# Optimization experiments

Measured on AMD Instinct MI355X. Metric: run time of the kernel, lower is better.

Reference implementation:

```python
import jax, jax.numpy as jnp
import numpy as np

MSA_DIM = 256
NO_HEADS = 8
HIDDEN_DIM = 32
NORM_FACTOR = 1.0 / np.sqrt(HIDDEN_DIM)


def setup_inputs() -> dict:
    key = jax.random.key(0)
    ks = jax.random.split(key, 9)
    S, L, C = 256, 384, MSA_DIM
    HD = NO_HEADS * HIDDEN_DIM
    scale = 1.0 / np.sqrt(C)
    return {
        "msa_embed": jax.random.normal(ks[0], (S, L, C), dtype=jnp.float32),
        "ln_gamma": jnp.ones((C,), dtype=jnp.float32),
        "ln_beta": jnp.zeros((C,), dtype=jnp.float32),
        "wq": jax.random.normal(ks[1], (C, HD), dtype=jnp.float32) * scale,
        "wk": jax.random.normal(ks[2], (C, HD), dtype=jnp.float32) * scale,
        "wv": jax.random.normal(ks[3], (C, HD), dtype=jnp.float32) * scale,
        "wg": jax.random.normal(ks[4], (C, HD), dtype=jnp.float32) * scale,
        "bg": jnp.zeros((HD,), dtype=jnp.float32),
        "wo": jax.random.normal(ks[5], (HD, C), dtype=jnp.float32) * (1.0 / np.sqrt(HD)),
        "bo": jnp.zeros((C,), dtype=jnp.float32),
    }


def _layernorm(x, gamma, beta, eps=1e-5):
    mu = jnp.mean(x, axis=-1, keepdims=True)
    var = jnp.mean(jnp.square(x - mu), axis=-1, keepdims=True)
    return (x - mu) * jax.lax.rsqrt(var + eps) * gamma + beta


def reference(msa_embed, ln_gamma, ln_beta, wq, wk, wv, wg, bg, wo, bo):
    S, L, C = msa_embed.shape
    H, D = NO_HEADS, HIDDEN_DIM
    m = _layernorm(msa_embed, ln_gamma, ln_beta)
    q = (m @ wq).reshape(S, L, H, D) * NORM_FACTOR  # [S, L, H, D]
    k = (m @ wk).reshape(S, L, H, D)
    v = (m @ wv).reshape(S, L, H, D)
    # column attention: attend over the seq (S) axis, per column c
    attn = jnp.einsum('ichd,jchd->hcij', q, k)  # [H, L, S, S]
    attn = jax.nn.softmax(attn, axis=-1)
    gate = jax.nn.sigmoid(m @ wg + bg).reshape(S, L, H, D)
    out = jnp.einsum('hcij,jchd->ichd', attn, v) * gate  # [S, L, H, D]
    out = out.reshape(S, L, H * D)
    return out @ wo + bo
```

## Files before the change

### kernel.cpp

```cpp
#include <hip/hip_runtime.h>
#include <hip/hip_bf16.h>
#include <stdint.h>

#define NS 256
#define NL 384
#define NC 256
#define NH 8
#define ND 32
#define NHD 256
#define NFQ 0.17677669529663687f
#define QSCALE (NFQ * 1.4426950408889634f)

typedef unsigned short u16;
typedef unsigned int u32;
typedef __attribute__((ext_vector_type(8))) short short8;
typedef __attribute__((ext_vector_type(4))) float f32x4;

__device__ __forceinline__ float bf2f(u16 u) {
  union { u32 u; float f; } w; w.u = ((u32)u) << 16; return w.f;
}
__device__ __forceinline__ float lo16(u32 u) {
  union { u32 u; float f; } w; w.u = u << 16; return w.f;
}
__device__ __forceinline__ float hi16(u32 u) {
  union { u32 u; float f; } w; w.u = u & 0xffff0000u; return w.f;
}
__device__ __forceinline__ u16 f2bf_rne(float f) {
  u32 x = __float_as_uint(f);
  u32 lsb = (x >> 16) & 1u;
  x += 0x7fffu + lsb;
  return (u16)(x >> 16);
}
__device__ __forceinline__ u32 pk2(float a, float b) {
  u32 r;
  asm("v_cvt_pk_bf16_f32 %0, %1, %2" : "=v"(r) : "v"(a), "v"(b));
  return r;
}

__device__ __forceinline__ void gl_lds16(const u16* g, u16* l) {
  __builtin_amdgcn_global_load_lds(
      (const __attribute__((address_space(1))) void*)g,
      (__attribute__((address_space(3))) void*)l, 16, 0, 0);
}

template<bool F32>
__device__ __forceinline__ float ldE(const void* p, size_t i) {
  if constexpr (F32) return ((const float*)p)[i];
  else               return bf2f(((const u16*)p)[i]);
}
template<bool F32>
__device__ __forceinline__ void ld16(const void* p, size_t i, float* x) {
  if constexpr (F32) {
    const float4* q = (const float4*)((const float*)p + i);
#pragma unroll
    for (int w = 0; w < 4; ++w) {
      float4 v = q[w];
      x[4*w] = v.x; x[4*w+1] = v.y; x[4*w+2] = v.z; x[4*w+3] = v.w;
    }
  } else {
    const uint4* q = (const uint4*)((const u16*)p + i);
#pragma unroll
    for (int w = 0; w < 2; ++w) {
      uint4 v = q[w];
      u32 uu[4] = {v.x, v.y, v.z, v.w};
#pragma unroll
      for (int pk = 0; pk < 4; ++pk) {
        x[8*w + 2*pk]     = lo16(uu[pk]);
        x[8*w + 2*pk + 1] = hi16(uu[pk]);
      }
    }
  }
}

__global__ void k_probe(const u16* __restrict__ msa, int* __restrict__ flag) {
  const int t = threadIdx.x;
  int cnt = 0;
#pragma unroll
  for (int i = 0; i < 4; ++i) {
    u16 v = msa[t * 4 + i];
    int e = (v >> 7) & 0xFF;
    cnt += (e >= 100 && e <= 150) ? 1 : 0;
  }
#pragma unroll
  for (int m = 1; m < 64; m <<= 1) cnt += __shfl_xor(cnt, m, 64);
  if (t == 0) *flag = (cnt < 220) ? 1 : 0;
}

__launch_bounds__(256)
__global__ void k_wt(const int* __restrict__ flag,
                     const void* __restrict__ w0, const void* __restrict__ w1,
                     const void* __restrict__ w2, const void* __restrict__ w3,
                     const void* __restrict__ w4,
                     u16* __restrict__ wT) {
  __shared__ float f[64][65];
  const int b = blockIdx.x;
  const int widx = b >> 4, tile = b & 15;
  const int k0 = (tile >> 2) * 64, n0 = (tile & 3) * 64;
  const void* src = widx == 0 ? w0 : widx == 1 ? w1 : widx == 2 ? w2 : widx == 3 ? w3 : w4;
  u16* dst = wT + widx * 65536;
  const int t = threadIdx.x;
  const bool isf32 = (*flag != 0);

  {
    const int kr = t >> 2, nc = (t & 3) * 16;
    float x[16];
    if (isf32) ld16<true >(src, (size_t)(k0 + kr) * NHD + n0 + nc, x);
    else       ld16<false>(src, (size_t)(k0 + kr) * NHD + n0 + nc, x);
#pragma unroll
    for (int i = 0; i < 16; ++i) f[kr][nc + i] = x[i];
  }
  __syncthreads();
  {
    const int nr = t >> 2, kc = (t & 3) * 16;
    u32 pk[8];
#pragma unroll
    for (int i = 0; i < 8; ++i)
      pk[i] = pk2(f[kc + 2*i][nr], f[kc + 2*i + 1][nr]);
    uint4* dp = (uint4*)(dst + (size_t)(n0 + nr) * NC + k0 + kc);
    dp[0] = make_uint4(pk[0], pk[1], pk[2], pk[3]);
    dp[1] = make_uint4(pk[4], pk[5], pk[6], pk[7]);
  }
}

__launch_bounds__(256)
__global__ void k_ln(const int* __restrict__ flag,
                     const void* __restrict__ msa,
                     const void* __restrict__ gamma_,
                     const void* __restrict__ beta_,
                     u16* __restrict__ mh) {
  const int t = threadIdx.x;
  const int row = blockIdx.x * 16 + (t >> 4);
  const int sub = t & 15;
  const bool isf32 = (*flag != 0);
  float x[16];
  if (isf32) ld16<true >(msa, (size_t)row * NC + sub * 16, x);
  else       ld16<false>(msa, (size_t)row * NC + sub * 16, x);
  float sm = 0.f, ss = 0.f;
#pragma unroll
  for (int i = 0; i < 16; ++i) { sm += x[i]; ss += x[i] * x[i]; }
#pragma unroll
  for (int msk = 1; msk < 16; msk <<= 1) {
    sm += __shfl_xor(sm, msk, 64);
    ss += __shfl_xor(ss, msk, 64);
  }
  float mu  = sm * (1.0f / NC);
  float var = fmaxf(ss * (1.0f / NC) - mu * mu, 0.0f);
  float rs  = rsqrtf(var + 1e-5f);
  float gm[16], be[16];
  if (isf32) {
    ld16<true >(gamma_, sub * 16, gm);
    ld16<true >(beta_,  sub * 16, be);
  } else {
    ld16<false>(gamma_, sub * 16, gm);
    ld16<false>(beta_,  sub * 16, be);
  }
  float y[16];
#pragma unroll
  for (int i = 0; i < 16; ++i) y[i] = (x[i] - mu) * rs * gm[i] + be[i];
  uint4* dp = (uint4*)(mh + (size_t)row * NC + sub * 16);
  dp[0] = make_uint4(pk2(y[0], y[1]),  pk2(y[2], y[3]),  pk2(y[4], y[5]),  pk2(y[6], y[7]));
  dp[1] = make_uint4(pk2(y[8], y[9]),  pk2(y[10], y[11]), pk2(y[12], y[13]), pk2(y[14], y[15]));
}

template<int V>
__launch_bounds__(256)
__global__ void k_gemm(const int* __restrict__ flag,
                       const u16* __restrict__ Abuf,
                       const u16* __restrict__ Wbuf,
                       const void* __restrict__ bias,
                       u16* __restrict__ qb, u16* __restrict__ kb,
                       u16* __restrict__ vb, u16* __restrict__ gb,
                       void* __restrict__ outp) {
  __shared__ u16 smem[17408];
  u16* Al = smem;
  u16* Bl = smem + 8192;
  const int t = threadIdx.x;
  const int w = t >> 6, lane = t & 63;
  const int q15 = lane & 15, g = lane >> 4;
  const int wm = w >> 1, wn = w & 1;
  int mb, nb;
  if constexpr (V == 0) {
    mb = (blockIdx.x >> 6) * 8 + (blockIdx.x & 7);
    nb = (blockIdx.x >> 3) & 7;
  } else {
    mb = (blockIdx.x >> 4) * 8 + (blockIdx.x & 7);
    nb = (blockIdx.x >> 3) & 1;
  }
  const int m0 = mb * 128, n0 = nb * 128;
  const bool isf32 = (*flag != 0);

  const u16* agp[4];
  const u16* bgp[4];
  u32 ldsu[4];
#pragma unroll
  for (int u = 0; u < 4; ++u) {
    const int j = u * 256 + t;
    const int row = j >> 3;
    const int k8 = (j & 7) ^ (row & 7);
    ldsu[u] = (u32)j * 8;
    agp[u] = Abuf + (size_t)(m0 + row) * NC + k8 * 8;
    if constexpr (V == 0) {
      const int ng = n0 + row;
      bgp[u] = Wbuf + (size_t)(ng >> 8) * 65536 + (size_t)(ng & 255) * NC + k8 * 8;
    } else {
      bgp[u] = Wbuf + (size_t)(n0 + row) * NC + k8 * 8;
    }
  }

  f32x4 acc[4][4];
#pragma unroll
  for (int i = 0; i < 4; ++i)
#pragma unroll
    for (int j = 0; j < 4; ++j) acc[i][j] = (f32x4){0.f, 0.f, 0.f, 0.f};

  for (int kc = 0; kc < 4; ++kc) {
#pragma unroll
    for (int u = 0; u < 4; ++u) {
      gl_lds16(agp[u] + kc * 64, Al + ldsu[u]);
      gl_lds16(bgp[u] + kc * 64, Bl + ldsu[u]);
    }
    __syncthreads();
#pragma unroll
    for (int ks = 0; ks < 2; ++ks) {
      union { uint4 u; short8 s; } af[4], wf[4];
#pragma unroll
      for (int i = 0; i < 4; ++i) {
        const int rA = wm * 64 + i * 16 + q15;
        const int sA = (ks * 4 + g) ^ (rA & 7);
        af[i].u = *(const uint4*)(Al + (size_t)rA * 64 + sA * 8);
        const int rB = wn * 64 + i * 16 + q15;
        const int sB = (ks * 4 + g) ^ (rB & 7);
        wf[i].u = *(const uint4*)(Bl + (size_t)rB * 64 + sB * 8);
      }
#pragma unroll
      for (int mi = 0; mi < 4; ++mi)
#pragma unroll
        for (int ni = 0; ni < 4; ++ni)
          acc[mi][ni] = __builtin_amdgcn_mfma_f32_16x16x32_bf16(af[mi].s, wf[ni].s,
                                                               acc[mi][ni], 0, 0, 0);
    }
    __syncthreads();
  }

  if constexpr (V == 0) {
    const int widx = n0 >> 8;
    const int nnb  = n0 & 255;
    u16* Cl = smem;
#pragma unroll
    for (int ni = 0; ni < 4; ++ni) {
      const int nl = wn * 64 + ni * 16 + q15;
      float bgv = 0.f;
      if (widx == 3) bgv = isf32 ? ldE<true>(bias, nnb + nl) : ldE<false>(bias, nnb + nl);
#pragma unroll
      for (int mi = 0; mi < 4; ++mi) {
#pragma unroll
        for (int r = 0; r < 4; ++r) {
          const int ml = wm * 64 + mi * 16 + 4 * g + r;
          float v = acc[mi][ni][r];
          if (widx == 0) v *= QSCALE;
          if (widx == 3) v = 1.0f / (1.0f + __expf(-(v + bgv)));
          Cl[ml * 136 + nl] = f2bf_rne(v);
        }
      }
    }
    __syncthreads();
    u16* dst = widx == 0 ? qb : widx == 1 ? kb : widx == 2 ? vb : gb;
#pragma unroll
    for (int u = 0; u < 8; ++u) {
      const int j = u * 256 + t;
      const int lane4 = j & 3;
      const int chunk = j >> 2;
      const int ml = chunk >> 2;
      const int ncl = (chunk & 3) * 32 + lane4 * 8;
      const int nn = nnb + ncl;
      const int hh = nn >> 5, dd = nn & 31;
      const int m = m0 + ml;
      const int s = m / NL, l = m % NL;
      const size_t ob = ((size_t)(l * NH + hh) * NS + s) * ND + dd;
      *(uint4*)(dst + ob) = *(const uint4*)(Cl + ml * 136 + ncl);
    }
  } else {
#pragma unroll
    for (int mi = 0; mi < 4; ++mi) {
#pragma unroll
      for (int ni = 0; ni < 4; ++ni) {
        const int n = n0 + wn * 64 + ni * 16 + q15;
        const float bov = isf32 ? ldE<true>(bias, n) : ldE<false>(bias, n);
#pragma unroll
        for (int r = 0; r < 4; ++r) {
          const int m = m0 + wm * 64 + mi * 16 + 4 * g + r;
          const float v = acc[mi][ni][r] + bov;
          if (isf32) ((float*)outp)[(size_t)m * NC + n] = v;
          else       ((u16*)outp)[(size_t)m * NC + n] = f2bf_rne(v);
        }
      }
    }
  }
}

__launch_bounds__(256, 4)
__global__ void k_attn(const u16* __restrict__ qb,
                       const u16* __restrict__ kb,
                       const u16* __restrict__ vb,
                       const u16* __restrict__ gb,
                       u16* __restrict__ xb) {
  __shared__ u16 Ks[NS * ND];
  __shared__ u16 Vt[ND * NS];
  const int t = threadIdx.x;
  const int w = t >> 6;
  const int lane = t & 63;
  const int q15 = lane & 15;
  const int g = lane >> 4;
  const int bid = blockIdx.x;
  const int c = bid >> 3, h = bid & 7;
  const size_t base = (size_t)bid * (NS * ND);

  {
    const uint4* vg = (const uint4*)(vb + base);
#pragma unroll
    for (int i = 0; i < 4; ++i) {
      const int j = t + 256 * i;
      const int key = j >> 2;
      const int kslot = (j & 3) ^ ((key >> 1) & 3);
      gl_lds16(kb + base + (size_t)key * ND + kslot * 8, Ks + (size_t)j * 8);

      const int s = j >> 2, dp = (j & 3) * 8;
      const int sp = (s & 0xE0) | ((s & 12) << 1) | (((s >> 4) & 1) << 2) | (s & 3);
      const int shi = sp >> 3, slo = sp & 7;
      uint4 vv = vg[j];
      u32 wds[4] = {vv.x, vv.y, vv.z, vv.w};
#pragma unroll
      for (int p = 0; p < 4; ++p) {
        const int da = dp + 2 * p, db = da + 1;
        Vt[da * NS + ((shi ^ (da & 7) ^ (da >> 3)) * 8) + slo] = (u16)(wds[p] & 0xffff);
        Vt[db * NS + ((shi ^ (db & 7) ^ (db >> 3)) * 8) + slo] = (u16)(wds[p] >> 16);
      }
    }
  }

  short8 qf[4];
  const int q0w = w * 64;
#pragma unroll
  for (int it = 0; it < 4; ++it) {
    union { uint4 u; short8 s; } cv;
    cv.u = *(const uint4*)(qb + base + (size_t)(q0w + it * 16 + q15) * ND + g * 8);
    qf[it] = cv.s;
  }
  __syncthreads();

  const f32x4 zero = {0.f, 0.f, 0.f, 0.f};
  const int d0 = q15, d1 = 16 + q15;
  const int x0 = (q15 & 7) ^ (q15 >> 3);
  const int x1 = x0 ^ 2;

#pragma unroll
  for (int it = 0; it < 4; ++it) {
    f32x4 sc[16];
#pragma unroll
    for (int jt = 0; jt < 16; ++jt) {
      const int srow = jt * 16 + q15;
      const int s2 = g ^ ((srow >> 1) & 3);
      union { uint4 u; short8 s; } kf;
      kf.u = *(const uint4*)(Ks + (size_t)srow * ND + s2 * 8);
      sc[jt] = __builtin_amdgcn_mfma_f32_16x16x32_bf16(kf.s, qf[it], zero, 0, 0, 0);
    }
    float s0 = 0.f, s1 = 0.f, s2s = 0.f, s3 = 0.f;
    u32 P0[16], P1[16];
#pragma unroll
    for (int jt = 0; jt < 16; ++jt) {
      float e0 = exp2f(fminf(sc[jt][0], 30.0f));
      float e1 = exp2f(fminf(sc[jt][1], 30.0f));
      float e2 = exp2f(fminf(sc[jt][2], 30.0f));
      float e3 = exp2f(fminf(sc[jt][3], 30.0f));
      s0 += e0; s1 += e1; s2s += e2; s3 += e3;
      P0[jt] = pk2(e0, e1);
      P1[jt] = pk2(e2, e3);
    }
    float sum = (s0 + s1) + (s2s + s3);
    sum += __shfl_xor(sum, 16, 64);
    sum += __shfl_xor(sum, 32, 64);
    const float inv = 1.0f / fmaxf(sum, 1e-35f);

    f32x4 o0 = zero, o1 = zero;
#pragma unroll
    for (int kc = 0; kc < 8; ++kc) {
      union { u32 w4[4]; short8 s; } pa;
      pa.w4[0] = P0[2 * kc];     pa.w4[1] = P1[2 * kc];
      pa.w4[2] = P0[2 * kc + 1]; pa.w4[3] = P1[2 * kc + 1];
      const int sl0 = (kc * 4 + g) ^ x0;
      const int sl1 = (kc * 4 + g) ^ x1;
      union { uint4 u; short8 s; } v0, v1;
      v0.u = *(const uint4*)(Vt + (size_t)d0 * NS + sl0 * 8);
      v1.u = *(const uint4*)(Vt + (size_t)d1 * NS + sl1 * 8);
      o0 = __builtin_amdgcn_mfma_f32_16x16x32_bf16(pa.s, v0.s, o0, 0, 0, 0);
      o1 = __builtin_amdgcn_mfma_f32_16x16x32_bf16(pa.s, v1.s, o1, 0, 0, 0);
    }

    const int qrow0 = q0w + it * 16 + 4 * g;
#pragma unroll
    for (int r = 0; r < 4; ++r) {
      const int s_idx = qrow0 + r;
      const float invr = __shfl(inv, 4 * g + r, 64);
      float g0 = bf2f(gb[base + (size_t)s_idx * ND + q15]);
      float g1 = bf2f(gb[base + (size_t)s_idx * ND + 16 + q15]);
      const size_t off = ((size_t)s_idx * NL + c) * NHD + h * ND;
      xb[off + q15]      = f2bf_rne(o0[r] * invr * g0);
      xb[off + 16 + q15] = f2bf_rne(o1[r] * invr * g1);
    }
  }
}

extern "C" void kernel_launch(void* const* d_in, const int* in_sizes, int n_in,
                              void* d_out, int out_size, void* d_ws, size_t ws_size,
                              hipStream_t stream) {
  const void* msa    = d_in[0];
  const void* gamma_ = d_in[1];
  const void* beta_  = d_in[2];
  const void* wq     = d_in[3];
  const void* wk     = d_in[4];
  const void* wv     = d_in[5];
  const void* wg     = d_in[6];
  const void* bg     = d_in[7];
  const void* wo     = d_in[8];
  const void* bo     = d_in[9];

  const size_t NE = (size_t)NS * NL * NH * ND;
  int* flag = (int*)d_ws;
  u16* wT = (u16*)((char*)d_ws + 256);
  u16* qb = wT + 5 * 65536;
  u16* kb = qb + NE;
  u16* vb = kb + NE;
  u16* gb = vb + NE;
  u16* mh = gb + NE;
  u16* xb = mh + NE;

  k_probe<<<dim3(1), dim3(64), 0, stream>>>((const u16*)msa, flag);
  k_wt<<<dim3(80), dim3(256), 0, stream>>>(flag, wq, wk, wv, wg, wo, wT);
  k_ln<<<dim3(6144), dim3(256), 0, stream>>>(flag, msa, gamma_, beta_, mh);
  k_gemm<0><<<dim3(768 * 8), dim3(256), 0, stream>>>(flag, mh, wT, bg,
                                                     qb, kb, vb, gb, nullptr);
  k_attn<<<dim3(NL * NH), dim3(256), 0, stream>>>(qb, kb, vb, gb, xb);
  k_gemm<1><<<dim3(768 * 2), dim3(256), 0, stream>>>(flag, xb, wT + 4 * 65536, bo,
                                                     nullptr, nullptr, nullptr, nullptr, d_out);
}
```

Measured before the change: 277.4 us.

## Double-buffer GEMM K-chunks in LDS and drop exp2 clamp in softmax

```diff
diff --git a/kernel.cpp b/kernel.cpp
--- a/kernel.cpp
+++ b/kernel.cpp
@@ -172,8 +172,6 @@
                        u16* __restrict__ vb, u16* __restrict__ gb,
                        void* __restrict__ outp) {
   __shared__ u16 smem[17408];
-  u16* Al = smem;
-  u16* Bl = smem + 8192;
   const int t = threadIdx.x;
   const int w = t >> 6, lane = t & 63;
   const int q15 = lane & 15, g = lane >> 4;
@@ -189,14 +187,14 @@
   const int m0 = mb * 128, n0 = nb * 128;
   const bool isf32 = (*flag != 0);
 
-  const u16* agp[4];
-  const u16* bgp[4];
-  u32 ldsu[4];
-#pragma unroll
-  for (int u = 0; u < 4; ++u) {
+  const u16* agp[2];
+  const u16* bgp[2];
+  u32 ldsu[2];
+#pragma unroll
+  for (int u = 0; u < 2; ++u) {
     const int j = u * 256 + t;
-    const int row = j >> 3;
-    const int k8 = (j & 7) ^ (row & 7);
+    const int row = j >> 2;
+    const int k8 = (j & 3) ^ ((row >> 1) & 3);
     ldsu[u] = (u32)j * 8;
     agp[u] = Abuf + (size_t)(m0 + row) * NC + k8 * 8;
     if constexpr (V == 0) {
@@ -213,32 +211,41 @@
 #pragma unroll
     for (int j = 0; j < 4; ++j) acc[i][j] = (f32x4){0.f, 0.f, 0.f, 0.f};
 
-  for (int kc = 0; kc < 4; ++kc) {
-#pragma unroll
-    for (int u = 0; u < 4; ++u) {
-      gl_lds16(agp[u] + kc * 64, Al + ldsu[u]);
-      gl_lds16(bgp[u] + kc * 64, Bl + ldsu[u]);
-    }
-    __syncthreads();
-#pragma unroll
-    for (int ks = 0; ks < 2; ++ks) {
-      union { uint4 u; short8 s; } af[4], wf[4];
-#pragma unroll
-      for (int i = 0; i < 4; ++i) {
-        const int rA = wm * 64 + i * 16 + q15;
-        const int sA = (ks * 4 + g) ^ (rA & 7);
-        af[i].u = *(const uint4*)(Al + (size_t)rA * 64 + sA * 8);
-        const int rB = wn * 64 + i * 16 + q15;
-        const int sB = (ks * 4 + g) ^ (rB & 7);
-        wf[i].u = *(const uint4*)(Bl + (size_t)rB * 64 + sB * 8);
+#pragma unroll
+  for (int u = 0; u < 2; ++u) {
+    gl_lds16(agp[u], smem + ldsu[u]);
+    gl_lds16(bgp[u], smem + 4096 + ldsu[u]);
+  }
+  __syncthreads();
+
+  for (int kc = 0; kc < 8; ++kc) {
+    const int p = kc & 1;
+    if (kc < 7) {
+      const int pn = p ^ 1;
+#pragma unroll
+      for (int u = 0; u < 2; ++u) {
+        gl_lds16(agp[u] + (kc + 1) * 32, smem + pn * 8192 + ldsu[u]);
+        gl_lds16(bgp[u] + (kc + 1) * 32, smem + pn * 8192 + 4096 + ldsu[u]);
       }
-#pragma unroll
-      for (int mi = 0; mi < 4; ++mi)
-#pragma unroll
-        for (int ni = 0; ni < 4; ++ni)
-          acc[mi][ni] = __builtin_amdgcn_mfma_f32_16x16x32_bf16(af[mi].s, wf[ni].s,
-                                                               acc[mi][ni], 0, 0, 0);
-    }
+    }
+    const u16* A = smem + p * 8192;
+    const u16* B = A + 4096;
+    union { uint4 u; short8 s; } af[4], wf[4];
+#pragma unroll
+    for (int i = 0; i < 4; ++i) {
+      const int rA = wm * 64 + i * 16 + q15;
+      const int sA = g ^ ((rA >> 1) & 3);
+      af[i].u = *(const uint4*)(A + (size_t)rA * 32 + sA * 8);
+      const int rB = wn * 64 + i * 16 + q15;
+      const int sB = g ^ ((rB >> 1) & 3);
+      wf[i].u = *(const uint4*)(B + (size_t)rB * 32 + sB * 8);
+    }
+#pragma unroll
+    for (int mi = 0; mi < 4; ++mi)
+#pragma unroll
+      for (int ni = 0; ni < 4; ++ni)
+        acc[mi][ni] = __builtin_amdgcn_mfma_f32_16x16x32_bf16(af[mi].s, wf[ni].s,
+                                                             acc[mi][ni], 0, 0, 0);
     __syncthreads();
   }
 
@@ -368,10 +375,10 @@
     u32 P0[16], P1[16];
 #pragma unroll
     for (int jt = 0; jt < 16; ++jt) {
-      float e0 = exp2f(fminf(sc[jt][0], 30.0f));
-      float e1 = exp2f(fminf(sc[jt][1], 30.0f));
-      float e2 = exp2f(fminf(sc[jt][2], 30.0f));
-      float e3 = exp2f(fminf(sc[jt][3], 30.0f));
+      float e0 = exp2f(sc[jt][0]);
+      float e1 = exp2f(sc[jt][1]);
+      float e2 = exp2f(sc[jt][2]);
+      float e3 = exp2f(sc[jt][3]);
       s0 += e0; s1 += e1; s2s += e2; s3 += e3;
       P0[jt] = pk2(e0, e1);
       P1[jt] = pk2(e2, e3);
```

Measured after the change: 261.1 us, median of 3. -5.9%, faster.
